# Kernel tuning notes

Hardware: AMD Instinct MI355X
Metric: run time of the kernel (lower is better)

## Reference

```python
import jax, jax.numpy as jnp
import numpy as np

K_WORDS = 256
RHO = 0.01
COUNT_EPS = 1e-4   # 0.0001 in the torch code
NORM_EPS = 1e-12   # F.normalize default eps


def _l2_normalize(v, axis):
    n = jnp.linalg.norm(v, axis=axis, keepdims=True)
    return v / jnp.maximum(n, NORM_EPS)


def setup_inputs() -> dict:
    key = jax.random.key(0)
    k1, k2 = jax.random.split(key)
    x = jax.random.normal(k1, (8, 2048, 64, 64), dtype=jnp.float32)
    centroid = jax.random.normal(k2, (K_WORDS, 2048), dtype=jnp.float32)
    return {"x": x, "centroid": centroid}


def reference(x, centroid):
    # x: [B, C, H, W], centroid: [K, C]. Everything on x is detached in the original.
    x = jax.lax.stop_gradient(x)
    B, C, H, W = x.shape

    # cosine similarity via L2-normalize + 1x1 conv (== einsum over channels)
    x_norm = _l2_normalize(x, axis=1)              # [B, C, H, W]
    w_norm = _l2_normalize(centroid, axis=1)       # [K, C]
    logits = jnp.einsum('bchw,kc->bkhw', x_norm, w_norm)
    x_corr = jax.nn.softmax(logits, axis=1)        # [B, K, H, W]

    x_label = jnp.argmax(x_corr, axis=1)           # [B, H, W]
    onehot = jax.nn.one_hot(x_label, K_WORDS, dtype=x.dtype)  # [B, H, W, K]
    y_word = jnp.sum(onehot, axis=(1, 2)) > 0      # [B, K] bool
    x_hist = jnp.sum(x_corr, axis=(2, 3), keepdims=True)      # [B, K, 1, 1]

    # EMA centroid update: normalized one-hot assignment matrix times features
    xx = jnp.transpose(x, (0, 2, 3, 1)).reshape(-1, C)        # [N, C], N = B*H*W
    yy = onehot.reshape(-1, K_WORDS)                           # [N, K]
    yy = yy / (jnp.sum(yy, axis=0) + COUNT_EPS)                # per-word normalize
    ctr = yy.T @ xx                                            # [K, C]
    new_centroid = RHO * ctr + (1.0 - RHO) * centroid

    # NOTE: the original forward returns (x_corr, x_hist, y_word) (its `x_label`
    # variable is actually the softmax map returned first by _cosine); the centroid
    # update is a stateful side effect, returned here explicitly.
    return x_corr, x_hist, y_word, new_centroid
```

## Files before the change

### kernel.cpp

```cpp
#include <hip/hip_runtime.h>

typedef __attribute__((ext_vector_type(8))) short short8;
typedef __attribute__((ext_vector_type(4))) float f32x4;
typedef __attribute__((ext_vector_type(4))) unsigned int u32x4;

#define C_DIM 2048
#define KW 256
#define HW_DIM 4096

__device__ __forceinline__ short f2bf(float f) {
    unsigned u = __builtin_bit_cast(unsigned, f);
    unsigned r = (u + 0x7fffu + ((u >> 16) & 1u)) >> 16;
    return (short)r;
}

__global__ __launch_bounds__(256) void k1_prep(const float* __restrict__ centroid,
                                               short* __restrict__ wt,
                                               float* __restrict__ xhist,
                                               int* __restrict__ counts) {
    const int row = blockIdx.x, t = threadIdx.x;
    const float* src = centroid + row * C_DIM;
    float v[8]; float ss = 0.f;
#pragma unroll
    for (int i = 0; i < 8; ++i) { v[i] = src[t + 256 * i]; ss += v[i] * v[i]; }
#pragma unroll
    for (int off = 1; off < 64; off <<= 1) ss += __shfl_xor(ss, off);
    __shared__ float red[4];
    if ((t & 63) == 0) red[t >> 6] = ss;
    __syncthreads();
    const float tot = red[0] + red[1] + red[2] + red[3];
    const float inv = 1.0f / fmaxf(sqrtf(tot), 1e-12f);
#pragma unroll
    for (int i = 0; i < 8; ++i) {
        const int c = t + 256 * i;
        const int idx = ((((c >> 6) * 2 + ((c >> 5) & 1)) * 4 + ((c >> 3) & 3)) * 256 + row) * 8 + (c & 7);
        wt[idx] = f2bf(v[i] * inv);
    }
    if (row == 0) {
        for (int i = t; i < 2048; i += 256) { xhist[i] = 0.f; counts[i] = 0; }
    }
}

__global__ __launch_bounds__(256, 2) void k2_main(const float* __restrict__ x,
                                                  const short* __restrict__ wt,
                                                  float* __restrict__ xcorr,
                                                  float* __restrict__ xhist,
                                                  int* __restrict__ labels,
                                                  int* __restrict__ counts) {
    __shared__ float sf[2][64 * 64];
    __shared__ short bfr[8 * 64 * 8];
    __shared__ float ssred[4][64];
    __shared__ float invn[64];
    __shared__ float wmax[4][64];
    __shared__ int   warg[4][64];
    __shared__ float wred[4][64];
    __shared__ float Sn[64];

    const int t = threadIdx.x;
    const int w = t >> 6, l = t & 63;
    const int p = l & 15, g = l >> 4;
    const int n0 = blockIdx.x * 64;
    const int b = n0 >> 12, hw0 = n0 & 4095;
    const float* xb = x + (size_t)b * C_DIM * HW_DIM + hw0;

    f32x4 acc[4][4];
#pragma unroll
    for (int i = 0; i < 4; ++i)
#pragma unroll
        for (int j = 0; j < 4; ++j) acc[i][j] = (f32x4)0.f;

    float ss = 0.f;
    int cur = 0;

#pragma unroll
    for (int q = 0; q < 4; ++q) {
        const int row = 4 * w + 16 * q + (l >> 4);
        const float* gsrc = xb + (size_t)row * HW_DIM + (l & 15) * 4;
        float* ldst = &sf[0][(4 * w + 16 * q) * 64];
        __builtin_amdgcn_global_load_lds(
            (const __attribute__((address_space(1))) unsigned int*)gsrc,
            (__attribute__((address_space(3))) unsigned int*)ldst, 16, 0, 0);
    }
    asm volatile("s_waitcnt vmcnt(0)" ::: "memory");
    __syncthreads();

#pragma unroll 1
    for (int cc = 0; cc < 32; ++cc) {
        const int cb = cc * 64;
        short8 af[2][4];
#pragma unroll
        for (int ks = 0; ks < 2; ++ks)
#pragma unroll
            for (int mf = 0; mf < 4; ++mf)
                af[ks][mf] = *(const short8*)(wt + (((size_t)(cc * 2 + ks) * 4 + g) * 256 + (w * 64 + mf * 16 + p)) * 8);
        __builtin_amdgcn_sched_barrier(0);
        if (cc + 1 < 32) {
#pragma unroll
            for (int q = 0; q < 4; ++q) {
                const int row = 4 * w + 16 * q + (l >> 4);
                const float* gsrc = xb + (size_t)(cb + 64 + row) * HW_DIM + (l & 15) * 4;
                float* ldst = &sf[cur ^ 1][(4 * w + 16 * q) * 64];
                __builtin_amdgcn_global_load_lds(
                    (const __attribute__((address_space(1))) unsigned int*)gsrc,
                    (__attribute__((address_space(3))) unsigned int*)ldst, 16, 0, 0);
            }
        }
        __builtin_amdgcn_sched_barrier(0);
        float tv[16];
#pragma unroll
        for (int j = 0; j < 16; ++j) {
            tv[j] = sf[cur][(16 * w + j) * 64 + l];
            ss += tv[j] * tv[j];
        }
        short8 pk0, pk1;
#pragma unroll
        for (int j = 0; j < 8; ++j) { pk0[j] = f2bf(tv[j]); pk1[j] = f2bf(tv[8 + j]); }
        *(short8*)(&bfr[((2 * w + 0) * 64 + l) * 8]) = pk0;
        *(short8*)(&bfr[((2 * w + 1) * 64 + l) * 8]) = pk1;
        asm volatile("s_waitcnt lgkmcnt(0)" ::: "memory");
        __builtin_amdgcn_sched_barrier(0);
        __builtin_amdgcn_s_barrier();
#pragma unroll
        for (int ks = 0; ks < 2; ++ks) {
            short8 bf[4];
#pragma unroll
            for (int nf = 0; nf < 4; ++nf)
                bf[nf] = *(const short8*)(&bfr[((ks * 4 + g) * 64 + nf * 16 + p) * 8]);
#pragma unroll
            for (int mf = 0; mf < 4; ++mf)
#pragma unroll
                for (int nf = 0; nf < 4; ++nf)
                    acc[mf][nf] = __builtin_amdgcn_mfma_f32_16x16x32_bf16(
                        af[ks][mf], bf[nf], acc[mf][nf], 0, 0, 0);
        }
        asm volatile("s_waitcnt vmcnt(0)" ::: "memory");
        __builtin_amdgcn_sched_barrier(0);
        __builtin_amdgcn_s_barrier();
        cur ^= 1;
    }

    ssred[w][l] = ss;
    __syncthreads();
    if (t < 64) {
        const float s = ssred[0][t] + ssred[1][t] + ssred[2][t] + ssred[3][t];
        invn[t] = 1.0f / fmaxf(sqrtf(s), 1e-12f);
    }
    __syncthreads();
    float inv[4];
#pragma unroll
    for (int nf = 0; nf < 4; ++nf) inv[nf] = invn[nf * 16 + p];

    float mx[4]; int ai[4];
#pragma unroll
    for (int nf = 0; nf < 4; ++nf) { mx[nf] = -3.0e38f; ai[nf] = 0; }
#pragma unroll
    for (int mf = 0; mf < 4; ++mf)
#pragma unroll
        for (int r = 0; r < 4; ++r) {
            const int k = w * 64 + mf * 16 + g * 4 + r;
#pragma unroll
            for (int nf = 0; nf < 4; ++nf) {
                const float v = acc[mf][nf][r] * inv[nf];
                if (v > mx[nf]) { mx[nf] = v; ai[nf] = k; }
            }
        }
#pragma unroll
    for (int off = 16; off <= 32; off <<= 1)
#pragma unroll
        for (int nf = 0; nf < 4; ++nf) {
            const float ov = __shfl_xor(mx[nf], off);
            const int   oi = __shfl_xor(ai[nf], off);
            if (ov > mx[nf] || (ov == mx[nf] && oi < ai[nf])) { mx[nf] = ov; ai[nf] = oi; }
        }
    if (l < 16) {
#pragma unroll
        for (int nf = 0; nf < 4; ++nf) { wmax[w][nf * 16 + l] = mx[nf]; warg[w][nf * 16 + l] = ai[nf]; }
    }
    __syncthreads();
    if (t < 64) {
        float m = wmax[0][t]; int a = warg[0][t];
#pragma unroll
        for (int ww = 1; ww < 4; ++ww) {
            const float om = wmax[ww][t]; const int oa = warg[ww][t];
            if (om > m || (om == m && oa < a)) { m = om; a = oa; }
        }
        labels[n0 + t] = a;
        atomicAdd(&counts[b * KW + a], 1);
    }

    float se[4] = {0.f, 0.f, 0.f, 0.f};
#pragma unroll
    for (int mf = 0; mf < 4; ++mf)
#pragma unroll
        for (int r = 0; r < 4; ++r)
#pragma unroll
            for (int nf = 0; nf < 4; ++nf)
                se[nf] += __expf(acc[mf][nf][r] * inv[nf]);
#pragma unroll
    for (int off = 16; off <= 32; off <<= 1)
#pragma unroll
        for (int nf = 0; nf < 4; ++nf) se[nf] += __shfl_xor(se[nf], off);
    if (l < 16) {
#pragma unroll
        for (int nf = 0; nf < 4; ++nf) wred[w][nf * 16 + l] = se[nf];
    }
    __syncthreads();
    if (t < 64) Sn[t] = wred[0][t] + wred[1][t] + wred[2][t] + wred[3][t];
    __syncthreads();

    float rs[4];
#pragma unroll
    for (int nf = 0; nf < 4; ++nf) rs[nf] = 1.0f / Sn[nf * 16 + p];

    float hist[4][4];
#pragma unroll
    for (int mf = 0; mf < 4; ++mf)
#pragma unroll
        for (int r = 0; r < 4; ++r) hist[mf][r] = 0.f;
#pragma unroll
    for (int mf = 0; mf < 4; ++mf)
#pragma unroll
        for (int r = 0; r < 4; ++r) {
            const int k = w * 64 + mf * 16 + g * 4 + r;
            float* orow = xcorr + ((size_t)(b * KW + k) << 12) + hw0;
#pragma unroll
            for (int nf = 0; nf < 4; ++nf) {
                const float pr = __expf(acc[mf][nf][r] * inv[nf]) * rs[nf];
                orow[nf * 16 + p] = pr;
                hist[mf][r] += pr;
            }
        }
#pragma unroll
    for (int off = 1; off <= 8; off <<= 1)
#pragma unroll
        for (int mf = 0; mf < 4; ++mf)
#pragma unroll
            for (int r = 0; r < 4; ++r) hist[mf][r] += __shfl_xor(hist[mf][r], off);
    if (p == 0) {
#pragma unroll
        for (int mf = 0; mf < 4; ++mf)
#pragma unroll
            for (int r = 0; r < 4; ++r)
                unsafeAtomicAdd(&xhist[b * KW + w * 64 + mf * 16 + g * 4 + r], hist[mf][r]);
    }
}

__global__ __launch_bounds__(256, 2) void k3_ctr(const float* __restrict__ x,
                                                 const int* __restrict__ labels,
                                                 float* __restrict__ partial4) {
    __shared__ int lab[1024];
    const int t = threadIdx.x;
    const int w = t >> 6, l = t & 63;
    const int p = l & 15, g = l >> 4;
    const int cc = blockIdx.x & 15;
    const int pg = (blockIdx.x >> 4) & 3;
    const int b  = blockIdx.x >> 6;
    ((int4*)lab)[t] = ((const int4*)(labels + b * HW_DIM + pg * 1024))[t];
    __syncthreads();

    const int c0 = cc * 128 + w * 32 + p;
    const int c1 = c0 + 16;
    const float* xr0 = x + ((size_t)b * C_DIM + c0) * HW_DIM + pg * 1024;
    const float* xr1 = x + ((size_t)b * C_DIM + c1) * HW_DIM + pg * 1024;

    f32x4 accA[16], accB[16];
#pragma unroll
    for (int mf = 0; mf < 16; ++mf) { accA[mf] = (f32x4)0.f; accB[mf] = (f32x4)0.f; }

    float4 a0 = *(const float4*)(xr0 + g * 8);
    float4 a1 = *(const float4*)(xr0 + g * 8 + 4);
    float4 e0 = *(const float4*)(xr1 + g * 8);
    float4 e1 = *(const float4*)(xr1 + g * 8 + 4);

#pragma unroll 1
    for (int px0 = 0; px0 < 1024; px0 += 32) {
        const int4 L0 = *(const int4*)(&lab[px0 + g * 8]);
        const int4 L1 = *(const int4*)(&lab[px0 + g * 8 + 4]);
        const int pxn = (px0 + 32 < 1024) ? (px0 + 32) : px0;
        float4 na0 = *(const float4*)(xr0 + pxn + g * 8);
        float4 na1 = *(const float4*)(xr0 + pxn + g * 8 + 4);
        float4 ne0 = *(const float4*)(xr1 + pxn + g * 8);
        float4 ne1 = *(const float4*)(xr1 + pxn + g * 8 + 4);

        short8 bfA, bfB;
        bfA[0] = f2bf(a0.x); bfA[1] = f2bf(a0.y); bfA[2] = f2bf(a0.z); bfA[3] = f2bf(a0.w);
        bfA[4] = f2bf(a1.x); bfA[5] = f2bf(a1.y); bfA[6] = f2bf(a1.z); bfA[7] = f2bf(a1.w);
        bfB[0] = f2bf(e0.x); bfB[1] = f2bf(e0.y); bfB[2] = f2bf(e0.z); bfB[3] = f2bf(e0.w);
        bfB[4] = f2bf(e1.x); bfB[5] = f2bf(e1.y); bfB[6] = f2bf(e1.z); bfB[7] = f2bf(e1.w);

        const int lj[8] = {L0.x, L0.y, L0.z, L0.w, L1.x, L1.y, L1.z, L1.w};
        unsigned bits[8];
#pragma unroll
        for (int j = 0; j < 8; ++j)
            bits[j] = ((lj[j] & 15) == p) ? (1u << (lj[j] >> 4)) : 0u;
        const unsigned cmb0 = bits[0] | (bits[1] << 16);
        const unsigned cmb1 = bits[2] | (bits[3] << 16);
        const unsigned cmb2 = bits[4] | (bits[5] << 16);
        const unsigned cmb3 = bits[6] | (bits[7] << 16);

#pragma unroll
        for (int mf = 0; mf < 16; ++mf) {
            u32x4 ar;
            ar[0] = ((cmb0 >> mf) & 0x00010001u) * 0x3F80u;
            ar[1] = ((cmb1 >> mf) & 0x00010001u) * 0x3F80u;
            ar[2] = ((cmb2 >> mf) & 0x00010001u) * 0x3F80u;
            ar[3] = ((cmb3 >> mf) & 0x00010001u) * 0x3F80u;
            const short8 af = __builtin_bit_cast(short8, ar);
            accA[mf] = __builtin_amdgcn_mfma_f32_16x16x32_bf16(af, bfA, accA[mf], 0, 0, 0);
            accB[mf] = __builtin_amdgcn_mfma_f32_16x16x32_bf16(af, bfB, accB[mf], 0, 0, 0);
        }
        a0 = na0; a1 = na1; e0 = ne0; e1 = ne1;
    }

    const int slice = b * 4 + pg;
#pragma unroll
    for (int mf = 0; mf < 16; ++mf)
#pragma unroll
        for (int r = 0; r < 4; ++r) {
            const size_t rowoff = (size_t)(slice * KW + mf * 16 + g * 4 + r) << 11;
            partial4[rowoff + c0] = accA[mf][r];
            partial4[rowoff + c1] = accB[mf][r];
        }
}

__global__ __launch_bounds__(256) void k4_final(const float* __restrict__ partial4,
                                                const int* __restrict__ counts,
                                                const float* __restrict__ centroid,
                                                float* __restrict__ out_c,
                                                float* __restrict__ y_word) {
    const int idx = blockIdx.x * 256 + threadIdx.x;
    const int k = idx >> 11, c = idx & 2047;
    float s = 0.f;
#pragma unroll
    for (int pi = 0; pi < 32; ++pi) s += partial4[((size_t)(pi * KW + k) << 11) + c];
    int cnt = 0;
#pragma unroll
    for (int bb = 0; bb < 8; ++bb) cnt += counts[bb * KW + k];
    const float ctr = s / ((float)cnt + 1e-4f);
    out_c[idx] = 0.01f * ctr + 0.99f * centroid[idx];
    if (idx < 2048) y_word[idx] = (counts[idx] > 0) ? 1.0f : 0.0f;
}

extern "C" void kernel_launch(void* const* d_in, const int* in_sizes, int n_in,
                              void* d_out, int out_size, void* d_ws, size_t ws_size,
                              hipStream_t stream) {
    const float* x        = (const float*)d_in[0];
    const float* centroid = (const float*)d_in[1];
    float* out   = (float*)d_out;
    float* xcorr = out;
    float* xhist = out + 8388608;
    float* yword = out + 8390656;
    float* outc  = out + 8392704;

    char* ws = (char*)d_ws;
    short* wt       = (short*)ws;
    int*   labels   = (int*)(ws + (1 << 20));
    int*   counts   = (int*)(ws + (1 << 20) + 131072);
    float* partial4 = (float*)(ws + (1 << 20) + 131072 + 8192);

    hipLaunchKernelGGL(k1_prep,  dim3(256),  dim3(256), 0, stream, centroid, wt, xhist, counts);
    hipLaunchKernelGGL(k2_main,  dim3(512),  dim3(256), 0, stream, x, wt, xcorr, xhist, labels, counts);
    hipLaunchKernelGGL(k3_ctr,   dim3(512),  dim3(256), 0, stream, x, labels, partial4);
    hipLaunchKernelGGL(k4_final, dim3(2048), dim3(256), 0, stream, partial4, counts, centroid, outc, yword);
}
```

Measured before the change: 154.9 us.

## Stage k3 feature loads through double-buffered LDS and store partials as bf16

The centroid-accumulation kernel now streams x tiles into a double-buffered, XOR-swizzled shared-memory buffer with direct global-to-LDS loads, replacing per-thread strided float4 register prefetch. This aims to get coalesced 64-pixel row loads and overlap the next tile's transfer with the MFMA work. The per-slice partial sums are also written and read as bf16 instead of fp32, halving the partial buffer traffic between k3 and k4 at the cost of extra rounding in the centroid result. The 64 KB of added LDS may limit occupancy relative to the launch bound of 2 blocks.

Result: faster. 141.7 us (median of 2 runs) (-8.5%).

```diff
diff --git a/kernel.cpp b/kernel.cpp
--- a/kernel.cpp
+++ b/kernel.cpp
@@ -12,6 +12,10 @@
     unsigned u = __builtin_bit_cast(unsigned, f);
     unsigned r = (u + 0x7fffu + ((u >> 16) & 1u)) >> 16;
     return (short)r;
+}
+
+__device__ __forceinline__ float bf2f(short s) {
+    return __builtin_bit_cast(float, ((unsigned)(unsigned short)s) << 16);
 }
 
 __global__ __launch_bounds__(256) void k1_prep(const float* __restrict__ centroid,
@@ -247,8 +251,9 @@
 
 __global__ __launch_bounds__(256, 2) void k3_ctr(const float* __restrict__ x,
                                                  const int* __restrict__ labels,
-                                                 float* __restrict__ partial4) {
+                                                 short* __restrict__ partial4) {
     __shared__ int lab[1024];
+    __shared__ float sf[2][128 * 64];
     const int t = threadIdx.x;
     const int w = t >> 6, l = t & 63;
     const int p = l & 15, g = l >> 4;
@@ -258,72 +263,101 @@
     ((int4*)lab)[t] = ((const int4*)(labels + b * HW_DIM + pg * 1024))[t];
     __syncthreads();
 
+    const float* xbase = x + ((size_t)b * C_DIM + cc * 128) * HW_DIM + pg * 1024;
+    const int dq_row = l >> 4;
+    const int dq_slot = l & 15;
+
+    f32x4 accA[16], accB[16];
+#pragma unroll
+    for (int mf = 0; mf < 16; ++mf) { accA[mf] = (f32x4)0.f; accB[mf] = (f32x4)0.f; }
+
+    const int r0 = w * 32 + p;
+    const int r1 = r0 + 16;
+
+#pragma unroll
+    for (int q = 0; q < 8; ++q) {
+        const int c_l = w * 32 + q * 4 + dq_row;
+        const int px4 = dq_slot ^ (c_l & 15);
+        const float* gsrc = xbase + (size_t)c_l * HW_DIM + px4 * 4;
+        float* ldst = &sf[0][(w * 32 + q * 4) * 64];
+        __builtin_amdgcn_global_load_lds(
+            (const __attribute__((address_space(1))) unsigned int*)gsrc,
+            (__attribute__((address_space(3))) unsigned int*)ldst, 16, 0, 0);
+    }
+
+#pragma unroll 1
+    for (int it = 0; it < 16; ++it) {
+        const int buf = it & 1;
+        if (it + 1 < 16) {
+#pragma unroll
+            for (int q = 0; q < 8; ++q) {
+                const int c_l = w * 32 + q * 4 + dq_row;
+                const int px4 = dq_slot ^ (c_l & 15);
+                const float* gsrc = xbase + (size_t)c_l * HW_DIM + (it + 1) * 64 + px4 * 4;
+                float* ldst = &sf[buf ^ 1][(w * 32 + q * 4) * 64];
+                __builtin_amdgcn_global_load_lds(
+                    (const __attribute__((address_space(1))) unsigned int*)gsrc,
+                    (__attribute__((address_space(3))) unsigned int*)ldst, 16, 0, 0);
+            }
+            asm volatile("s_waitcnt vmcnt(8)" ::: "memory");
+        } else {
+            asm volatile("s_waitcnt vmcnt(0)" ::: "memory");
+        }
+        __builtin_amdgcn_sched_barrier(0);
+#pragma unroll
+        for (int H = 0; H < 2; ++H) {
+            const int sE = ((H * 8 + g * 2) ^ p) * 4;
+            const int sO = ((H * 8 + g * 2 + 1) ^ p) * 4;
+            const float4 v0 = *(const float4*)&sf[buf][r0 * 64 + sE];
+            const float4 v1 = *(const float4*)&sf[buf][r0 * 64 + sO];
+            const float4 v2 = *(const float4*)&sf[buf][r1 * 64 + sE];
+            const float4 v3 = *(const float4*)&sf[buf][r1 * 64 + sO];
+            short8 bfA, bfB;
+            bfA[0] = f2bf(v0.x); bfA[1] = f2bf(v0.y); bfA[2] = f2bf(v0.z); bfA[3] = f2bf(v0.w);
+            bfA[4] = f2bf(v1.x); bfA[5] = f2bf(v1.y); bfA[6] = f2bf(v1.z); bfA[7] = f2bf(v1.w);
+            bfB[0] = f2bf(v2.x); bfB[1] = f2bf(v2.y); bfB[2] = f2bf(v2.z); bfB[3] = f2bf(v2.w);
+            bfB[4] = f2bf(v3.x); bfB[5] = f2bf(v3.y); bfB[6] = f2bf(v3.z); bfB[7] = f2bf(v3.w);
+
+            const int lb = it * 64 + H * 32 + g * 8;
+            const int4 L0 = *(const int4*)&lab[lb];
+            const int4 L1 = *(const int4*)&lab[lb + 4];
+            const int lj[8] = {L0.x, L0.y, L0.z, L0.w, L1.x, L1.y, L1.z, L1.w};
+            unsigned bits[8];
+#pragma unroll
+            for (int j = 0; j < 8; ++j)
+                bits[j] = ((lj[j] & 15) == p) ? (1u << (lj[j] >> 4)) : 0u;
+            const unsigned cmb0 = bits[0] | (bits[1] << 16);
+            const unsigned cmb1 = bits[2] | (bits[3] << 16);
+            const unsigned cmb2 = bits[4] | (bits[5] << 16);
+            const unsigned cmb3 = bits[6] | (bits[7] << 16);
+
+#pragma unroll
+            for (int mf = 0; mf < 16; ++mf) {
+                u32x4 ar;
+                ar[0] = ((cmb0 >> mf) & 0x00010001u) * 0x3F80u;
+                ar[1] = ((cmb1 >> mf) & 0x00010001u) * 0x3F80u;
+                ar[2] = ((cmb2 >> mf) & 0x00010001u) * 0x3F80u;
+                ar[3] = ((cmb3 >> mf) & 0x00010001u) * 0x3F80u;
+                const short8 af = __builtin_bit_cast(short8, ar);
+                accA[mf] = __builtin_amdgcn_mfma_f32_16x16x32_bf16(af, bfA, accA[mf], 0, 0, 0);
+                accB[mf] = __builtin_amdgcn_mfma_f32_16x16x32_bf16(af, bfB, accB[mf], 0, 0, 0);
+            }
+        }
+    }
+
+    const int slice = b * 4 + pg;
     const int c0 = cc * 128 + w * 32 + p;
-    const int c1 = c0 + 16;
-    const float* xr0 = x + ((size_t)b * C_DIM + c0) * HW_DIM + pg * 1024;
-    const float* xr1 = x + ((size_t)b * C_DIM + c1) * HW_DIM + pg * 1024;
-
-    f32x4 accA[16], accB[16];
-#pragma unroll
-    for (int mf = 0; mf < 16; ++mf) { accA[mf] = (f32x4)0.f; accB[mf] = (f32x4)0.f; }
-
-    float4 a0 = *(const float4*)(xr0 + g * 8);
-    float4 a1 = *(const float4*)(xr0 + g * 8 + 4);
-    float4 e0 = *(const float4*)(xr1 + g * 8);
-    float4 e1 = *(const float4*)(xr1 + g * 8 + 4);
-
-#pragma unroll 1
-    for (int px0 = 0; px0 < 1024; px0 += 32) {
-        const int4 L0 = *(const int4*)(&lab[px0 + g * 8]);
-        const int4 L1 = *(const int4*)(&lab[px0 + g * 8 + 4]);
-        const int pxn = (px0 + 32 < 1024) ? (px0 + 32) : px0;
-        float4 na0 = *(const float4*)(xr0 + pxn + g * 8);
-        float4 na1 = *(const float4*)(xr0 + pxn + g * 8 + 4);
-        float4 ne0 = *(const float4*)(xr1 + pxn + g * 8);
-        float4 ne1 = *(const float4*)(xr1 + pxn + g * 8 + 4);
-
-        short8 bfA, bfB;
-        bfA[0] = f2bf(a0.x); bfA[1] = f2bf(a0.y); bfA[2] = f2bf(a0.z); bfA[3] = f2bf(a0.w);
-        bfA[4] = f2bf(a1.x); bfA[5] = f2bf(a1.y); bfA[6] = f2bf(a1.z); bfA[7] = f2bf(a1.w);
-        bfB[0] = f2bf(e0.x); bfB[1] = f2bf(e0.y); bfB[2] = f2bf(e0.z); bfB[3] = f2bf(e0.w);
-        bfB[4] = f2bf(e1.x); bfB[5] = f2bf(e1.y); bfB[6] = f2bf(e1.z); bfB[7] = f2bf(e1.w);
-
-        const int lj[8] = {L0.x, L0.y, L0.z, L0.w, L1.x, L1.y, L1.z, L1.w};
-        unsigned bits[8];
-#pragma unroll
-        for (int j = 0; j < 8; ++j)
-            bits[j] = ((lj[j] & 15) == p) ? (1u << (lj[j] >> 4)) : 0u;
-        const unsigned cmb0 = bits[0] | (bits[1] << 16);
-        const unsigned cmb1 = bits[2] | (bits[3] << 16);
-        const unsigned cmb2 = bits[4] | (bits[5] << 16);
-        const unsigned cmb3 = bits[6] | (bits[7] << 16);
-
-#pragma unroll
-        for (int mf = 0; mf < 16; ++mf) {
-            u32x4 ar;
-            ar[0] = ((cmb0 >> mf) & 0x00010001u) * 0x3F80u;
-            ar[1] = ((cmb1 >> mf) & 0x00010001u) * 0x3F80u;
-            ar[2] = ((cmb2 >> mf) & 0x00010001u) * 0x3F80u;
-            ar[3] = ((cmb3 >> mf) & 0x00010001u) * 0x3F80u;
-            const short8 af = __builtin_bit_cast(short8, ar);
-            accA[mf] = __builtin_amdgcn_mfma_f32_16x16x32_bf16(af, bfA, accA[mf], 0, 0, 0);
-            accB[mf] = __builtin_amdgcn_mfma_f32_16x16x32_bf16(af, bfB, accB[mf], 0, 0, 0);
-        }
-        a0 = na0; a1 = na1; e0 = ne0; e1 = ne1;
-    }
-
-    const int slice = b * 4 + pg;
 #pragma unroll
     for (int mf = 0; mf < 16; ++mf)
 #pragma unroll
         for (int r = 0; r < 4; ++r) {
             const size_t rowoff = (size_t)(slice * KW + mf * 16 + g * 4 + r) << 11;
-            partial4[rowoff + c0] = accA[mf][r];
-            partial4[rowoff + c1] = accB[mf][r];
-        }
-}
-
-__global__ __launch_bounds__(256) void k4_final(const float* __restrict__ partial4,
+            partial4[rowoff + c0] = f2bf(accA[mf][r]);
+            partial4[rowoff + c0 + 16] = f2bf(accB[mf][r]);
+        }
+}
+
+__global__ __launch_bounds__(256) void k4_final(const short* __restrict__ partial4,
                                                 const int* __restrict__ counts,
                                                 const float* __restrict__ centroid,
                                                 float* __restrict__ out_c,
@@ -332,7 +366,7 @@
     const int k = idx >> 11, c = idx & 2047;
     float s = 0.f;
 #pragma unroll
-    for (int pi = 0; pi < 32; ++pi) s += partial4[((size_t)(pi * KW + k) << 11) + c];
+    for (int pi = 0; pi < 32; ++pi) s += bf2f(partial4[((size_t)(pi * KW + k) << 11) + c]);
     int cnt = 0;
 #pragma unroll
     for (int bb = 0; bb < 8; ++bb) cnt += counts[bb * KW + k];
@@ -356,7 +390,7 @@
     short* wt       = (short*)ws;
     int*   labels   = (int*)(ws + (1 << 20));
     int*   counts   = (int*)(ws + (1 << 20) + 131072);
-    float* partial4 = (float*)(ws + (1 << 20) + 131072 + 8192);
+    short* partial4 = (short*)(ws + (1 << 20) + 131072 + 8192);
 
     hipLaunchKernelGGL(k1_prep,  dim3(256),  dim3(256), 0, stream, centroid, wt, xhist, counts);
     hipLaunchKernelGGL(k2_main,  dim3(512),  dim3(256), 0, stream, x, wt, xcorr, xhist, labels, counts);
```
